# Kernel tuning notes

Measured on AMD Instinct MI355X. Metric: run time of the kernel, lower is better.

## Reference

```python
import jax, jax.numpy as jnp
import numpy as np

# cfg constants (from init_kwargs)
RBF_START = 0.0
RBF_END = 10.0
RBF_STEPS = 32
ENERGY_SCALE = 1.0
EPS = 1e-10

L, R, E, F, P = 64, 4096, 32, 64, 8


def setup_inputs() -> dict:
    key = jax.random.key(0)
    ks = jax.random.split(key, 6)
    return {
        "lig_feat": jax.random.normal(ks[0], (L, E, F), dtype=jnp.float32),
        "rec_feat": jax.random.normal(ks[1], (R, E, F), dtype=jnp.float32),
        "lig_coords": jax.random.normal(ks[2], (P, L, 3), dtype=jnp.float32),
        "rec_coord": jax.random.normal(ks[3], (R, 3), dtype=jnp.float32),
        "weight": jax.random.normal(ks[4], (), dtype=jnp.float32),
        "bias": jax.random.normal(ks[5], (), dtype=jnp.float32),
    }


def reference(lig_feat, rec_feat, lig_coords, rec_coord, weight, bias):
    # attention coefficients: [L, R, E]
    atn = jnp.einsum('lef,ref->lre', lig_feat, rec_feat)
    mu = jnp.linspace(RBF_START, RBF_END, RBF_STEPS, dtype=jnp.float32)  # [E]
    sigma = (RBF_START - RBF_END) / RBF_STEPS

    def energy(lig_coord):  # lig_coord: [L, 3]
        # cdist_diff: eps added per-coordinate before sum, as in the torch code
        diff = lig_coord[:, None, :] - rec_coord[None, :, :]      # [L, R, 3]
        dists = jnp.sqrt(((diff * diff) + EPS).sum(-1))            # [L, R]
        z = (dists[..., None] - mu) / sigma                        # [L, R, E]
        rbfs = jnp.exp(-(z * z))
        return (atn * rbfs * ENERGY_SCALE).sum()

    Us = jax.vmap(energy)(lig_coords)  # [P]
    # ScaleOutput
    return Us * weight + bias
```

## Files before the change

### kernel.cpp

```cpp
#include <hip/hip_runtime.h>

#define NL 64
#define NR 4096
#define NE 32
#define NF 64
#define NP 8

#define DSCALE 3.8435917081166390f
#define MUSTEP 1.2398683f
#define EPS3   3e-10f

typedef _Float16 f16x8 __attribute__((ext_vector_type(8)));
typedef __fp16   h16x2 __attribute__((ext_vector_type(2)));
typedef float    f32x4 __attribute__((ext_vector_type(4)));

#define NBLK 1024
#define PART_B (NL * NE * NF * 2)

#define REC_B   0
#define COORD_B 16384
#define CSTRIDE 144
#define LDS_SZ  (16384 + 9216)

__global__ __launch_bounds__(256)
void ff_prep(const float* __restrict__ lig_feat, void* __restrict__ ws) {
    const int tid = blockIdx.x * 256 + threadIdx.x;
    const float4 v = ((const float4*)lig_feat)[tid];
    union { h16x2 h[2]; uint2 u; } pk;
    pk.h[0] = __builtin_amdgcn_cvt_pkrtz(v.x, v.y);
    pk.h[1] = __builtin_amdgcn_cvt_pkrtz(v.z, v.w);
    ((uint2*)ws)[tid] = pk.u;
}

__global__ __launch_bounds__(256, 2)
void ff_main(const float* __restrict__ rec_feat,
             const float* __restrict__ lig_coords,
             const float* __restrict__ rec_coord,
             void* __restrict__ ws)
{
    __shared__ __align__(16) char smem[LDS_SZ];

    const int t    = threadIdx.x;
    const int bid  = blockIdx.x;
    const int rb   = bid & 255;
    const int eb   = bid >> 8;
    const int r0   = rb * 16;
    const int e0   = eb * 8;
    const int lane = t & 63;
    const int wv   = t >> 6;
    const int l0   = wv * 16;
    const int cn   = lane & 15;
    const int kg   = lane >> 4;

    const int srow = t >> 4, sfq = t & 15;
    const int rswz = (8 * sfq) ^ ((srow & 7) << 4);
    const float* recrow = &rec_feat[((r0 + srow) * NE + e0) * NF + sfq * 4];
    float4 h0[4], h1[4];
#pragma unroll
    for (int e = 0; e < 4; ++e) h0[e] = *(const float4*)(recrow + e * NF);
#pragma unroll
    for (int e = 0; e < 4; ++e) h1[e] = *(const float4*)(recrow + (e + 4) * NF);

#pragma unroll
    for (int j = 0; j < 6; ++j) {
        const int s = j * 256 + t;
        const int p = s / 192;
        const int rem = s - p * 192;
        const int l = rem / 3, c = rem - l * 3;
        *(float*)(smem + COORD_B + l * CSTRIDE + p * 16 + c * 4) = lig_coords[s];
    }
#pragma unroll
    for (int e = 0; e < 4; ++e) {
        union { h16x2 h[2]; uint2 u; } pk;
        pk.h[0] = __builtin_amdgcn_cvt_pkrtz(h0[e].x, h0[e].y);
        pk.h[1] = __builtin_amdgcn_cvt_pkrtz(h0[e].z, h0[e].w);
        *(uint2*)(smem + REC_B + e * 2048 + srow * 128 + rswz) = pk.u;
    }
    __syncthreads();

    const int rr = r0 + cn;
    const float rx = rec_coord[rr * 3 + 0];
    const float ry = rec_coord[rr * 3 + 1];
    const float rz = rec_coord[rr * 3 + 2];
    float ds[4][NP];
#pragma unroll
    for (int reg = 0; reg < 4; ++reg) {
        const int l = l0 + kg * 4 + reg;
#pragma unroll
        for (int p = 0; p < NP; ++p) {
            const float4 lc = *(const float4*)(smem + COORD_B + l * CSTRIDE + p * 16);
            const float dx = lc.x - rx, dy = lc.y - ry, dz = lc.z - rz;
            const float d2 = fmaf(dx, dx, fmaf(dy, dy, fmaf(dz, dz, EPS3)));
            ds[reg][p] = __builtin_amdgcn_sqrtf(d2) * DSCALE;
        }
    }

    const unsigned short* ligb =
        (const unsigned short*)ws + ((l0 + cn) * NE + e0) * NF + kg * 8;
    const int bsw = (cn & 7) << 4;
    const int b0o = REC_B + cn * 128 + ((kg * 16) ^ bsw);
    const int b1o = REC_B + cn * 128 + ((kg * 16 + 64) ^ bsw);

    float U[NP];
#pragma unroll
    for (int p = 0; p < NP; ++p) U[p] = 0.f;

    uint4 an0 = *(const uint4*)(ligb);
    uint4 an1 = *(const uint4*)(ligb + 32);

#pragma unroll
    for (int ee = 0; ee < 8; ++ee) {
        union { uint4 u; f16x8 v; } a0, a1;
        a0.u = an0;
        a1.u = an1;
        if (ee < 7) {
            an0 = *(const uint4*)(ligb + (ee + 1) * NF);
            an1 = *(const uint4*)(ligb + (ee + 1) * NF + 32);
        }
        const f16x8 b0 = *(const f16x8*)(smem + b0o + ee * 2048);
        const f16x8 b1 = *(const f16x8*)(smem + b1o + ee * 2048);
        f32x4 C = {0.f, 0.f, 0.f, 0.f};
        C = __builtin_amdgcn_mfma_f32_16x16x32_f16(a0.v, b0, C, 0, 0, 0);
        C = __builtin_amdgcn_mfma_f32_16x16x32_f16(a1.v, b1, C, 0, 0, 0);

        const float mu = (float)(e0 + ee) * MUSTEP;
#pragma unroll
        for (int reg = 0; reg < 4; ++reg) {
            const float a = C[reg];
#pragma unroll
            for (int p = 0; p < NP; ++p) {
                const float z = ds[reg][p] - mu;
                U[p] = fmaf(a, __builtin_amdgcn_exp2f(-(z * z)), U[p]);
            }
        }

        if (ee == 3) {
#pragma unroll
            for (int e = 0; e < 4; ++e) {
                union { h16x2 h[2]; uint2 u; } pk;
                pk.h[0] = __builtin_amdgcn_cvt_pkrtz(h1[e].x, h1[e].y);
                pk.h[1] = __builtin_amdgcn_cvt_pkrtz(h1[e].z, h1[e].w);
                *(uint2*)(smem + REC_B + (e + 4) * 2048 + srow * 128 + rswz) = pk.u;
            }
            __syncthreads();
        }
    }

#pragma unroll
    for (int p = 0; p < NP; ++p) {
        float v = U[p];
        for (int off = 32; off; off >>= 1) v += __shfl_down(v, off, 64);
        U[p] = v;
    }
    float* wred = (float*)(smem + COORD_B);
    if (lane == 0) {
#pragma unroll
        for (int p = 0; p < NP; ++p) wred[wv * 8 + p] = U[p];
    }
    __syncthreads();
    float* part = (float*)((char*)ws + PART_B);
    if (t < NP)
        part[t * NBLK + bid] = wred[t] + wred[8 + t] + wred[16 + t] + wred[24 + t];
}

__global__ __launch_bounds__(512)
void ff_fin(const void* __restrict__ ws,
            const float* __restrict__ w,
            const float* __restrict__ b,
            float* __restrict__ out) {
    const float* part = (const float*)((const char*)ws + PART_B);
    const int t = threadIdx.x, lane = t & 63, p = t >> 6;
    float s = 0.f;
#pragma unroll
    for (int j = 0; j < NBLK / 256; ++j) {
        const float4 v = *(const float4*)&part[p * NBLK + j * 256 + lane * 4];
        s += (v.x + v.y) + (v.z + v.w);
    }
    for (int off = 32; off; off >>= 1) s += __shfl_down(s, off, 64);
    if (lane == 0) out[p] = fmaf(s, w[0], b[0]);
}

extern "C" void kernel_launch(void* const* d_in, const int* in_sizes, int n_in,
                              void* d_out, int out_size, void* d_ws, size_t ws_size,
                              hipStream_t stream) {
    const float* lig_feat   = (const float*)d_in[0];
    const float* rec_feat   = (const float*)d_in[1];
    const float* lig_coords = (const float*)d_in[2];
    const float* rec_coord  = (const float*)d_in[3];
    const float* weight     = (const float*)d_in[4];
    const float* bias       = (const float*)d_in[5];
    float* out = (float*)d_out;

    hipLaunchKernelGGL(ff_prep, dim3(128), dim3(256), 0, stream, lig_feat, d_ws);
    hipLaunchKernelGGL(ff_main, dim3(NBLK), dim3(256), 0, stream,
                       rec_feat, lig_coords, rec_coord, d_ws);
    hipLaunchKernelGGL(ff_fin, dim3(1), dim3(512), 0, stream,
                       d_ws, weight, bias, out);
}
```

Measured before the change: 31.89 us.

## Halve per-block E range, pack distances in fp16, raise occupancy to four blocks

The E dimension is split over twice as many blocks (2048, four E values each). This drops the mid-loop second rec_feat LDS stage and its barrier, and shrinks LDS to about 17.5 KB. Scaled distances are stored as packed fp16 registers instead of 32 floats, and the launch bound asks for four blocks per CU. The aim is more occupancy and latency hiding. In exchange, coordinates and rec_coord are reloaded per block, fp16 rounding of distances can add error in the RBF exponent, and the lig-feature prefetch pipelining is removed.

```diff
diff --git a/kernel.cpp b/kernel.cpp
--- a/kernel.cpp
+++ b/kernel.cpp
@@ -14,29 +14,31 @@
 typedef __fp16   h16x2 __attribute__((ext_vector_type(2)));
 typedef float    f32x4 __attribute__((ext_vector_type(4)));
 
-#define NBLK 1024
+#define NBLK 2048
 #define PART_B (NL * NE * NF * 2)
 
 #define REC_B   0
-#define COORD_B 16384
+#define COORD_B 8192
+#define WRED_B  17408
 #define CSTRIDE 144
-#define LDS_SZ  (16384 + 9216)
+#define LDS_SZ  17536
 
 __global__ __launch_bounds__(256)
-void ff_prep(const float* __restrict__ lig_feat, void* __restrict__ ws) {
+void ff_prep(const float* __restrict__ lig_feat, unsigned short* __restrict__ lig16) {
     const int tid = blockIdx.x * 256 + threadIdx.x;
     const float4 v = ((const float4*)lig_feat)[tid];
     union { h16x2 h[2]; uint2 u; } pk;
     pk.h[0] = __builtin_amdgcn_cvt_pkrtz(v.x, v.y);
     pk.h[1] = __builtin_amdgcn_cvt_pkrtz(v.z, v.w);
-    ((uint2*)ws)[tid] = pk.u;
+    ((uint2*)lig16)[tid] = pk.u;
 }
 
-__global__ __launch_bounds__(256, 2)
-void ff_main(const float* __restrict__ rec_feat,
+__global__ __launch_bounds__(256, 4)
+void ff_main(const unsigned short* __restrict__ lig16,
+             const float* __restrict__ rec_feat,
              const float* __restrict__ lig_coords,
              const float* __restrict__ rec_coord,
-             void* __restrict__ ws)
+             float* __restrict__ part)
 {
     __shared__ __align__(16) char smem[LDS_SZ];
 
@@ -45,21 +47,12 @@
     const int rb   = bid & 255;
     const int eb   = bid >> 8;
     const int r0   = rb * 16;
-    const int e0   = eb * 8;
+    const int e0   = eb * 4;
     const int lane = t & 63;
     const int wv   = t >> 6;
     const int l0   = wv * 16;
     const int cn   = lane & 15;
     const int kg   = lane >> 4;
-
-    const int srow = t >> 4, sfq = t & 15;
-    const int rswz = (8 * sfq) ^ ((srow & 7) << 4);
-    const float* recrow = &rec_feat[((r0 + srow) * NE + e0) * NF + sfq * 4];
-    float4 h0[4], h1[4];
-#pragma unroll
-    for (int e = 0; e < 4; ++e) h0[e] = *(const float4*)(recrow + e * NF);
-#pragma unroll
-    for (int e = 0; e < 4; ++e) h1[e] = *(const float4*)(recrow + (e + 4) * NF);
 
 #pragma unroll
     for (int j = 0; j < 6; ++j) {
@@ -69,11 +62,15 @@
         const int l = rem / 3, c = rem - l * 3;
         *(float*)(smem + COORD_B + l * CSTRIDE + p * 16 + c * 4) = lig_coords[s];
     }
+    const int srow = t >> 4, sfq = t & 15;
+    const int rswz = (8 * sfq) ^ ((srow & 7) << 4);
+    const float* recrow = &rec_feat[((r0 + srow) * NE + e0) * NF + sfq * 4];
 #pragma unroll
     for (int e = 0; e < 4; ++e) {
+        const float4 v = *(const float4*)(recrow + e * NF);
         union { h16x2 h[2]; uint2 u; } pk;
-        pk.h[0] = __builtin_amdgcn_cvt_pkrtz(h0[e].x, h0[e].y);
-        pk.h[1] = __builtin_amdgcn_cvt_pkrtz(h0[e].z, h0[e].w);
+        pk.h[0] = __builtin_amdgcn_cvt_pkrtz(v.x, v.y);
+        pk.h[1] = __builtin_amdgcn_cvt_pkrtz(v.z, v.w);
         *(uint2*)(smem + REC_B + e * 2048 + srow * 128 + rswz) = pk.u;
     }
     __syncthreads();
@@ -82,21 +79,26 @@
     const float rx = rec_coord[rr * 3 + 0];
     const float ry = rec_coord[rr * 3 + 1];
     const float rz = rec_coord[rr * 3 + 2];
-    float ds[4][NP];
+    uint4 dsp[4];
 #pragma unroll
     for (int reg = 0; reg < 4; ++reg) {
         const int l = l0 + kg * 4 + reg;
+        float d[NP];
 #pragma unroll
         for (int p = 0; p < NP; ++p) {
             const float4 lc = *(const float4*)(smem + COORD_B + l * CSTRIDE + p * 16);
             const float dx = lc.x - rx, dy = lc.y - ry, dz = lc.z - rz;
             const float d2 = fmaf(dx, dx, fmaf(dy, dy, fmaf(dz, dz, EPS3)));
-            ds[reg][p] = __builtin_amdgcn_sqrtf(d2) * DSCALE;
+            d[p] = __builtin_amdgcn_sqrtf(d2) * DSCALE;
         }
+        union { h16x2 h[4]; uint4 u; } pk;
+#pragma unroll
+        for (int q = 0; q < 4; ++q)
+            pk.h[q] = __builtin_amdgcn_cvt_pkrtz(d[2 * q], d[2 * q + 1]);
+        dsp[reg] = pk.u;
     }
 
-    const unsigned short* ligb =
-        (const unsigned short*)ws + ((l0 + cn) * NE + e0) * NF + kg * 8;
+    const unsigned short* ligb = lig16 + ((l0 + cn) * NE + e0) * NF + kg * 8;
     const int bsw = (cn & 7) << 4;
     const int b0o = REC_B + cn * 128 + ((kg * 16) ^ bsw);
     const int b1o = REC_B + cn * 128 + ((kg * 16 + 64) ^ bsw);
@@ -105,18 +107,11 @@
 #pragma unroll
     for (int p = 0; p < NP; ++p) U[p] = 0.f;
 
-    uint4 an0 = *(const uint4*)(ligb);
-    uint4 an1 = *(const uint4*)(ligb + 32);
-
 #pragma unroll
-    for (int ee = 0; ee < 8; ++ee) {
+    for (int ee = 0; ee < 4; ++ee) {
         union { uint4 u; f16x8 v; } a0, a1;
-        a0.u = an0;
-        a1.u = an1;
-        if (ee < 7) {
-            an0 = *(const uint4*)(ligb + (ee + 1) * NF);
-            an1 = *(const uint4*)(ligb + (ee + 1) * NF + 32);
-        }
+        a0.u = *(const uint4*)(ligb + ee * NF);
+        a1.u = *(const uint4*)(ligb + ee * NF + 32);
         const f16x8 b0 = *(const f16x8*)(smem + b0o + ee * 2048);
         const f16x8 b1 = *(const f16x8*)(smem + b1o + ee * 2048);
         f32x4 C = {0.f, 0.f, 0.f, 0.f};
@@ -127,22 +122,13 @@
 #pragma unroll
         for (int reg = 0; reg < 4; ++reg) {
             const float a = C[reg];
+            union { uint4 u; __fp16 h[8]; } pk;
+            pk.u = dsp[reg];
 #pragma unroll
             for (int p = 0; p < NP; ++p) {
-                const float z = ds[reg][p] - mu;
-                U[p] = fmaf(a, __builtin_amdgcn_exp2f(-(z * z)), U[p]);
+                const float z = (float)pk.h[p] - mu;
+                U[p] = fmaf(a, __builtin_amdgcn_exp2f(fmaf(-z, z, 0.f)), U[p]);
             }
-        }
-
-        if (ee == 3) {
-#pragma unroll
-            for (int e = 0; e < 4; ++e) {
-                union { h16x2 h[2]; uint2 u; } pk;
-                pk.h[0] = __builtin_amdgcn_cvt_pkrtz(h1[e].x, h1[e].y);
-                pk.h[1] = __builtin_amdgcn_cvt_pkrtz(h1[e].z, h1[e].w);
-                *(uint2*)(smem + REC_B + (e + 4) * 2048 + srow * 128 + rswz) = pk.u;
-            }
-            __syncthreads();
         }
     }
 
@@ -152,23 +138,21 @@
         for (int off = 32; off; off >>= 1) v += __shfl_down(v, off, 64);
         U[p] = v;
     }
-    float* wred = (float*)(smem + COORD_B);
+    float* wred = (float*)(smem + WRED_B);
     if (lane == 0) {
 #pragma unroll
         for (int p = 0; p < NP; ++p) wred[wv * 8 + p] = U[p];
     }
     __syncthreads();
-    float* part = (float*)((char*)ws + PART_B);
     if (t < NP)
         part[t * NBLK + bid] = wred[t] + wred[8 + t] + wred[16 + t] + wred[24 + t];
 }
 
 __global__ __launch_bounds__(512)
-void ff_fin(const void* __restrict__ ws,
+void ff_fin(const float* __restrict__ part,
             const float* __restrict__ w,
             const float* __restrict__ b,
             float* __restrict__ out) {
-    const float* part = (const float*)((const char*)ws + PART_B);
     const int t = threadIdx.x, lane = t & 63, p = t >> 6;
     float s = 0.f;
 #pragma unroll
@@ -190,10 +174,12 @@
     const float* weight     = (const float*)d_in[4];
     const float* bias       = (const float*)d_in[5];
     float* out = (float*)d_out;
+    unsigned short* lig16 = (unsigned short*)d_ws;
+    float* part = (float*)((char*)d_ws + PART_B);
 
-    hipLaunchKernelGGL(ff_prep, dim3(128), dim3(256), 0, stream, lig_feat, d_ws);
+    hipLaunchKernelGGL(ff_prep, dim3(128), dim3(256), 0, stream, lig_feat, lig16);
     hipLaunchKernelGGL(ff_main, dim3(NBLK), dim3(256), 0, stream,
-                       rec_feat, lig_coords, rec_coord, d_ws);
+                       lig16, rec_feat, lig_coords, rec_coord, part);
     hipLaunchKernelGGL(ff_fin, dim3(1), dim3(512), 0, stream,
-                       d_ws, weight, bias, out);
+                       part, weight, bias, out);
 }
```

After: 30.67 us. -3.9%, faster.
